# Kernel optimization log

Hardware: AMD Instinct MI355X
Metric: run time of the kernel (lower is better)

Reference implementation:

```python
import jax, jax.numpy as jnp
import numpy as np

B, L, C = 256, 256, 128
HID, H = 128, 4
D = HID // H            # 32
NUM_LAYERS = 2
NEG_SLOPE = 0.2
LN_EPS = 1e-5


def setup_inputs() -> dict:
    key = jax.random.key(0)
    ks = jax.random.split(key, 16)
    E = 4096
    x = jax.random.normal(ks[0], (B, L, C), dtype=jnp.float32)
    edge_index = jax.random.randint(ks[1], (2, E), 0, C, dtype=jnp.int64)
    s_in = 1.0 / np.sqrt(L)
    s_h = 1.0 / np.sqrt(HID)
    return {
        "x": x,
        "edge_index": edge_index,
        "emb_W": jax.random.normal(ks[2], (L, HID), jnp.float32) * s_in,
        "emb_b": jnp.zeros((HID,), jnp.float32),
        "lin_l_W": jax.random.normal(ks[3], (NUM_LAYERS, HID, HID), jnp.float32) * s_h,
        "lin_l_b": jnp.zeros((NUM_LAYERS, HID), jnp.float32),
        "lin_r_W": jax.random.normal(ks[4], (NUM_LAYERS, HID, HID), jnp.float32) * s_h,
        "lin_r_b": jnp.zeros((NUM_LAYERS, HID), jnp.float32),
        "att": jax.random.normal(ks[5], (NUM_LAYERS, H, D), jnp.float32) * (1.0 / np.sqrt(D)),
        "gat_bias": jnp.zeros((NUM_LAYERS, HID), jnp.float32),
        "ln_gamma": jnp.ones((NUM_LAYERS, HID), jnp.float32),
        "ln_beta": jnp.zeros((NUM_LAYERS, HID), jnp.float32),
        "proj_W": jax.random.normal(ks[6], (HID, L), jnp.float32) * s_h,
        "proj_b": jnp.zeros((L,), jnp.float32),
    }


def _batch_edges(edge_index):
    # replicate single-graph edges per batch sample with node offsets, then add self loops
    E = edge_index.shape[1]
    off = jnp.repeat(jnp.arange(B, dtype=edge_index.dtype) * C, E)
    src = jnp.tile(edge_index[0], B) + off
    dst = jnp.tile(edge_index[1], B) + off
    loop = jnp.arange(B * C, dtype=edge_index.dtype)
    return jnp.concatenate([src, loop]), jnp.concatenate([dst, loop])


def _layer_norm(x, g, b):
    mu = jnp.mean(x, axis=-1, keepdims=True)
    var = jnp.mean(jnp.square(x - mu), axis=-1, keepdims=True)
    return (x - mu) * jax.lax.rsqrt(var + LN_EPS) * g + b


def _gatv2(x, src, dst, Wl, bl, Wr, br, a, bias):
    N = x.shape[0]
    xl = (x @ Wl + bl).reshape(N, H, D)   # source-side transform
    xr = (x @ Wr + br).reshape(N, H, D)   # target-side transform
    e = jax.nn.leaky_relu(xl[src] + xr[dst], NEG_SLOPE)   # (E', H, D)
    logits = jnp.einsum('ehd,hd->eh', e, a)               # (E', H)
    m = jax.ops.segment_max(logits, dst, num_segments=N)
    p = jnp.exp(logits - m[dst])
    s = jax.ops.segment_sum(p, dst, num_segments=N)
    alpha = p / (s[dst] + 1e-16)
    out = jax.ops.segment_sum(xl[src] * alpha[:, :, None], dst, num_segments=N)
    return out.reshape(N, HID) + bias, alpha


def reference(x, edge_index, emb_W, emb_b, lin_l_W, lin_l_b, lin_r_W, lin_r_b,
              att, gat_bias, ln_gamma, ln_beta, proj_W, proj_b):
    src, dst = _batch_edges(edge_index)
    # (B, L, C) -> nodes are channels: (B*C, L) -> embed to HID
    h = x.transpose(0, 2, 1).reshape(B * C, L) @ emb_W + emb_b
    alpha = None
    for i in range(NUM_LAYERS):
        new_h, alpha = _gatv2(h, src, dst, lin_l_W[i], lin_l_b[i],
                              lin_r_W[i], lin_r_b[i], att[i], gat_bias[i])
        new_h = jax.nn.elu(new_h)
        h = h + new_h
        h = _layer_norm(h, ln_gamma[i], ln_beta[i])
        # dropout: eval mode, identity
    # attention map (to_dense_adj semantics: adj[b, src%C, dst%C] = mean_h(alpha), then transpose)
    b_idx = src // C
    dense = jnp.zeros((B, C, C), x.dtype).at[b_idx, src % C, dst % C].add(alpha.mean(axis=-1))
    attn_map = dense.transpose(0, 2, 1)
    out = (h @ proj_W + proj_b).reshape(B, C, L).transpose(0, 2, 1)  # (B, L, C)
    return out, attn_map
```

## Files before the change

### kernel.cpp

```cpp
#include <hip/hip_runtime.h>
#include <hip/hip_fp16.h>
#include <math.h>

#define BB 256
#define LL 256
#define CC 128
#define HIDD 128
#define HH 4
#define DD 32
#define EE 4096
#define NN (BB*CC)
#define LN_EPS 1e-5f

typedef short bf16x8 __attribute__((ext_vector_type(8)));
typedef _Float16 f16x8 __attribute__((ext_vector_type(8)));
typedef float f32x4 __attribute__((ext_vector_type(4)));

__device__ __forceinline__ float red64(float p) {
    p += __shfl_xor(p, 32);
    p += __shfl_xor(p, 16);
    p += __shfl_xor(p, 8);
    p += __shfl_xor(p, 4);
    p += __shfl_xor(p, 2);
    p += __shfl_xor(p, 1);
    return p;
}
__device__ __forceinline__ unsigned bfr(float f) {
    unsigned x = __float_as_uint(f);
    return (x + 0x7FFFu + ((x >> 16) & 1u)) >> 16;
}
__device__ __forceinline__ unsigned pack2(float a, float b) { return bfr(a) | (bfr(b) << 16); }
__device__ __forceinline__ float b2f(unsigned u) { return __uint_as_float(u << 16); }

__device__ __forceinline__ void stage_bf16_rm(ushort* lds, const ushort* src, int ldm, int t) {
    #pragma unroll
    for (int i = 0; i < 8; ++i) {
        int flat = i*256 + t;
        int r = flat >> 4, c = flat & 15;
        uint4 pk = *(const uint4*)(src + (size_t)r*ldm + c*8);
        *(uint4*)&lds[((r*16) + (c ^ (r & 7)))*8] = pk;
    }
}
__device__ __forceinline__ void mfma_tile_128(const ushort* Als, const ushort* Bls,
                                              f32x4 acc[2][8], int w, int lane) {
    int mr = lane & 15, quad = lane >> 4;
    #pragma unroll
    for (int ks = 0; ks < 4; ++ks) {
        int ca = ks*4 + quad;
        bf16x8 a[2], b[8];
        #pragma unroll
        for (int mf = 0; mf < 2; ++mf) {
            int m = w*32 + mf*16 + mr;
            a[mf] = *(const bf16x8*)&Als[((m*16) + (ca ^ (m & 7)))*8];
        }
        #pragma unroll
        for (int nf = 0; nf < 8; ++nf) {
            int n = nf*16 + mr;
            b[nf] = *(const bf16x8*)&Bls[((n*16) + (ca ^ (n & 7)))*8];
        }
        #pragma unroll
        for (int mf = 0; mf < 2; ++mf)
            #pragma unroll
            for (int nf = 0; nf < 8; ++nf)
                acc[mf][nf] = __builtin_amdgcn_mfma_f32_16x16x32_bf16(a[mf], b[nf], acc[mf][nf], 0, 0, 0);
    }
}
#define ZERO_ACC(acc) { _Pragma("unroll") for (int i_=0;i_<2;++i_) { _Pragma("unroll") for (int j_=0;j_<8;++j_) acc[i_][j_] = (f32x4){0.f,0.f,0.f,0.f}; } }

__global__ __launch_bounds__(256) void prep_weights(const float* __restrict__ emb_W,
                                                    const float* __restrict__ lWl,
                                                    const float* __restrict__ lWr,
                                                    const float* __restrict__ pW,
                                                    const int* __restrict__ edge,
                                                    ushort* __restrict__ WembT,
                                                    ushort* __restrict__ WlrT,
                                                    ushort* __restrict__ WpT,
                                                    __half* __restrict__ mult_ds) {
    __shared__ int cnt[CC*CC];
    int t = threadIdx.x;
    if (blockIdx.x == 64) {
        for (int i = t; i < CC*CC; i += 256) cnt[i] = 0;
        __syncthreads();
        for (int j = t; j < EE; j += 256) {
            int s = edge[j], d = edge[EE + j];
            atomicAdd(&cnt[s*CC + d], 1);
        }
        __syncthreads();
        for (int o = t; o < CC*CC; o += 256) {
            int dstc = o >> 7, srcc = o & 127;
            int c = cnt[srcc*CC + dstc] + ((srcc == dstc) ? 1 : 0);
            mult_ds[o] = __float2half((float)c);
        }
        return;
    }
    int gid = blockIdx.x * 256 + t;
    float v[8];
    if (gid < 4096) {
        int f = gid >> 5, ch = gid & 31;
        #pragma unroll
        for (int j = 0; j < 8; ++j) v[j] = emb_W[(size_t)(ch*8 + j)*HIDD + f];
        uint4 pk; pk.x = pack2(v[0],v[1]); pk.y = pack2(v[2],v[3]);
        pk.z = pack2(v[4],v[5]); pk.w = pack2(v[6],v[7]);
        *(uint4*)&WembT[(size_t)f*LL + ch*8] = pk;
    } else if (gid < 12288) {
        int g = gid - 4096;
        int mat = g >> 11, f = (g >> 4) & 127, ch = g & 15;
        const float* src = ((mat & 1) ? lWr : lWl) + (size_t)(mat >> 1)*HIDD*HIDD;
        #pragma unroll
        for (int j = 0; j < 8; ++j) v[j] = src[(size_t)(ch*8 + j)*HIDD + f];
        uint4 pk; pk.x = pack2(v[0],v[1]); pk.y = pack2(v[2],v[3]);
        pk.z = pack2(v[4],v[5]); pk.w = pack2(v[6],v[7]);
        *(uint4*)&WlrT[(size_t)mat*HIDD*HIDD + (size_t)f*HIDD + ch*8] = pk;
    } else {
        int g = gid - 12288;
        int l = g >> 4, ch = g & 15;
        #pragma unroll
        for (int j = 0; j < 8; ++j) v[j] = pW[(size_t)(ch*8 + j)*LL + l];
        uint4 pk; pk.x = pack2(v[0],v[1]); pk.y = pack2(v[2],v[3]);
        pk.z = pack2(v[4],v[5]); pk.w = pack2(v[6],v[7]);
        *(uint4*)&WpT[(size_t)l*HIDD + ch*8] = pk;
    }
}

__global__ __launch_bounds__(256) void embed_mfma(const float* __restrict__ x,
                                                  const ushort* __restrict__ WembT,
                                                  const float* __restrict__ bias,
                                                  ushort* __restrict__ hout) {
    __shared__ __align__(16) ushort Als[128*16*8];
    __shared__ __align__(16) ushort Bls[128*16*8];
    int b = blockIdx.x;
    int t = threadIdx.x, lane = t & 63, w = t >> 6;
    f32x4 acc[2][8];
    ZERO_ACC(acc)
    #pragma unroll
    for (int kh = 0; kh < 2; ++kh) {
        if (kh) __syncthreads();
        const float4* x4 = (const float4*)(x + (size_t)b*LL*CC + (size_t)kh*128*CC);
        int rot = (t >> 3) & 3;
        #pragma unroll
        for (int i = 0; i < 8; ++i) {
            int flat = i*256 + t;
            int lp = flat >> 5, c4 = flat & 31;
            float4 v0 = x4[(size_t)(2*lp)*32 + c4];
            float4 v1 = x4[(size_t)(2*lp + 1)*32 + c4];
            int lc = lp >> 2, lh = lp & 3;
            #pragma unroll
            for (int j0 = 0; j0 < 4; ++j0) {
                int j = (j0 + rot) & 3;
                int c = c4*4 + j;
                unsigned pk = pack2(((const float*)&v0)[j], ((const float*)&v1)[j]);
                *(unsigned*)&Als[((c*16) + (lc ^ (c & 7)))*8 + lh*2] = pk;
            }
        }
        stage_bf16_rm(Bls, WembT + kh*128, LL, t);
        __syncthreads();
        mfma_tile_128(Als, Bls, acc, w, lane);
    }
    int mr = lane & 15, quad = lane >> 4;
    #pragma unroll
    for (int nf = 0; nf < 8; ++nf) {
        int f = nf*16 + mr;
        float bv = bias[f];
        #pragma unroll
        for (int mf = 0; mf < 2; ++mf)
            #pragma unroll
            for (int r = 0; r < 4; ++r) {
                int node = w*32 + mf*16 + quad*4 + r;
                hout[((size_t)b*CC + node)*HIDD + f] = (ushort)bfr(acc[mf][nf][r] + bv);
            }
    }
}

__global__ __launch_bounds__(256) void lin_mfma(const ushort* __restrict__ hmat,
                                                const ushort* __restrict__ WlT,
                                                const ushort* __restrict__ WrT,
                                                const float* __restrict__ bl,
                                                const float* __restrict__ br,
                                                __half* __restrict__ xlT,
                                                __half* __restrict__ xrT) {
    __shared__ __align__(16) ushort Als[128*16*8];
    __shared__ __align__(16) ushort Bls[128*16*8];
    int b = blockIdx.x;
    int t = threadIdx.x, lane = t & 63, w = t >> 6;
    int mr = lane & 15, quad = lane >> 4;
    stage_bf16_rm(Als, hmat + (size_t)b*CC*HIDD, HIDD, t);
    #pragma unroll
    for (int lr = 0; lr < 2; ++lr) {
        if (lr) __syncthreads();
        stage_bf16_rm(Bls, lr ? WrT : WlT, HIDD, t);
        __syncthreads();
        f32x4 acc[2][8];
        ZERO_ACC(acc)
        mfma_tile_128(Als, Bls, acc, w, lane);
        const float* bias = lr ? br : bl;
        __half* out = lr ? xrT : xlT;
        #pragma unroll
        for (int nf = 0; nf < 8; ++nf) {
            int f = nf*16 + mr;
            float bv = bias[f];
            int h = f >> 5, d = f & 31;
            #pragma unroll
            for (int mf = 0; mf < 2; ++mf)
                #pragma unroll
                for (int r = 0; r < 4; ++r) {
                    int node = w*32 + mf*16 + quad*4 + r;
                    out[(((size_t)b*HH + h)*CC + node)*DD + d] = __float2half(acc[mf][nf][r] + bv);
                }
        }
    }
}

__global__ __launch_bounds__(256, 4) void gat_fused(const __half* __restrict__ xl_h,
                                                    const __half* __restrict__ xr_h,
                                                    const __half* __restrict__ mult_ds,
                                                    const float* __restrict__ att,
                                                    __half* __restrict__ xagg,
                                                    __half* __restrict__ Pg) {
    __shared__ __align__(16) __half xl_lds[CC*DD];
    __shared__ __align__(16) __half xlT_swz[DD*16*8];
    __shared__ float Slq[CC];
    __shared__ float rpart[4][CC];
    __shared__ float spart[4][CC];

    int bh = blockIdx.x;
    int h = bh & 3, b = bh >> 2;
    int t = threadIdx.x;
    int sg = t >> 6, dl = t & 63;
    int dstA = dl, dstB = dl + 64;

    {
        const uint4* sp = (const uint4*)(xl_h + (size_t)bh * CC * DD);
        uint4* dp = (uint4*)xl_lds;
        dp[t] = sp[t];
        dp[t + 256] = sp[t + 256];
    }
    __half2 qa2[16];
    const float* ag = att + h*DD;
    #pragma unroll
    for (int c = 0; c < 8; ++c) {
        float4 av = *(const float4*)&ag[c*4];
        qa2[2*c+0] = __floats2half2_rn(0.4f*av.x, 0.4f*av.y);
        qa2[2*c+1] = __floats2half2_rn(0.4f*av.z, 0.4f*av.w);
    }
    __half2 xrA[16], xrB[16];
    float fSA, fSB;
    {
        uint4 XA[4], XB[4];
        const uint4* pa = (const uint4*)(xr_h + ((size_t)bh*CC + dstA)*DD);
        const uint4* pb = (const uint4*)(xr_h + ((size_t)bh*CC + dstB)*DD);
        #pragma unroll
        for (int c = 0; c < 4; ++c) { XA[c] = pa[c]; XB[c] = pb[c]; }
        const __half2* va = (const __half2*)XA;
        const __half2* vb = (const __half2*)XB;
        float sA = 0.f, sB = 0.f;
        #pragma unroll
        for (int i = 0; i < 16; ++i) {
            xrA[i] = va[i]; xrB[i] = vb[i];
            __half2 p = __hmul2(qa2[i], xrA[i]);
            sA += __low2float(p) + __high2float(p);
            __half2 q = __hmul2(qa2[i], xrB[i]);
            sB += __low2float(q) + __high2float(q);
        }
        fSA = 1.5f * sA; fSB = 1.5f * sB;
    }
    __syncthreads();

    if (t < CC) {
        uint4 R[4];
        const uint4* rp = (const uint4*)&xl_lds[t*DD];
        #pragma unroll
        for (int c = 0; c < 4; ++c) R[c] = rp[c];
        const __half2* rv = (const __half2*)R;
        __half2 s = __floats2half2_rn(0.f, 0.f);
        #pragma unroll
        for (int i = 0; i < 16; ++i) s = __hfma2(qa2[i], rv[i], s);
        Slq[t] = 1.5f * (__low2float(s) + __high2float(s));
    }
    for (int i = t; i < 512; i += 256) {
        int f = i & 31, c = i >> 5;
        __align__(16) __half v[8];
        #pragma unroll
        for (int e = 0; e < 8; ++e) v[e] = xl_lds[(c*8 + e)*DD + f];
        *(uint4*)&xlT_swz[((f*16) + (c ^ (f & 7)))*8] = *(uint4*)v;
    }
    __syncthreads();

    __half2 lvA[16], lvB[16];
    float pmA0 = -3.0e38f, pmA1 = pmA0, pmB0 = pmA0, pmB1 = pmA0;
    float lbufA = 0.f, lbufB = 0.f;
    #pragma unroll
    for (int j = 0; j < 32; ++j) {
        int src = sg*32 + j;
        uint4 R[4];
        const uint4* rp = (const uint4*)&xl_lds[src*DD];
        R[0] = rp[0]; R[1] = rp[1]; R[2] = rp[2]; R[3] = rp[3];
        float sl = Slq[src];
        const __half2* xv = (const __half2*)R;
        __half2 a0 = __floats2half2_rn(0.f,0.f), a1 = a0, a2 = a0, a3 = a0;
        __half2 b0 = a0, b1 = a0, b2 = a0, b3 = a0;
        #pragma unroll
        for (int q = 0; q < 4; ++q) {
            a0 = __hfma2(qa2[4*q+0], __habs2(__hadd2(xv[4*q+0], xrA[4*q+0])), a0);
            a1 = __hfma2(qa2[4*q+1], __habs2(__hadd2(xv[4*q+1], xrA[4*q+1])), a1);
            a2 = __hfma2(qa2[4*q+2], __habs2(__hadd2(xv[4*q+2], xrA[4*q+2])), a2);
            a3 = __hfma2(qa2[4*q+3], __habs2(__hadd2(xv[4*q+3], xrA[4*q+3])), a3);
            b0 = __hfma2(qa2[4*q+0], __habs2(__hadd2(xv[4*q+0], xrB[4*q+0])), b0);
            b1 = __hfma2(qa2[4*q+1], __habs2(__hadd2(xv[4*q+1], xrB[4*q+1])), b1);
            b2 = __hfma2(qa2[4*q+2], __habs2(__hadd2(xv[4*q+2], xrB[4*q+2])), b2);
            b3 = __hfma2(qa2[4*q+3], __habs2(__hadd2(xv[4*q+3], xrB[4*q+3])), b3);
        }
        __half2 tsA = __hadd2(__hadd2(a0, a1), __hadd2(a2, a3));
        __half2 tsB = __hadd2(__hadd2(b0, b1), __hadd2(b2, b3));
        float lA = (fSA + sl) + (__low2float(tsA) + __high2float(tsA));
        float lB = (fSB + sl) + (__low2float(tsB) + __high2float(tsB));
        if (j & 1) {
            pmA1 = fmaxf(pmA1, lA); pmB1 = fmaxf(pmB1, lB);
            lvA[j >> 1] = __floats2half2_rn(lbufA, lA);
            lvB[j >> 1] = __floats2half2_rn(lbufB, lB);
        } else {
            pmA0 = fmaxf(pmA0, lA); pmB0 = fmaxf(pmB0, lB);
            lbufA = lA; lbufB = lB;
        }
    }
    rpart[sg][dstA] = fmaxf(pmA0, pmA1);
    rpart[sg][dstB] = fmaxf(pmB0, pmB1);
    __syncthreads();
    float mA = fmaxf(fmaxf(rpart[0][dstA], rpart[1][dstA]),
                     fmaxf(rpart[2][dstA], rpart[3][dstA]));
    float mB = fmaxf(fmaxf(rpart[0][dstB], rpart[1][dstB]),
                     fmaxf(rpart[2][dstB], rpart[3][dstB]));

    uint4 MAr[4], MBr[4];
    {
        const uint4* ma = (const uint4*)(mult_ds + (size_t)dstA*CC + sg*32);
        const uint4* mb = (const uint4*)(mult_ds + (size_t)dstB*CC + sg*32);
        #pragma unroll
        for (int c = 0; c < 4; ++c) { MAr[c] = ma[c]; MBr[c] = mb[c]; }
    }
    const __half* multA = (const __half*)MAr;
    const __half* multB = (const __half*)MBr;

    float sA0 = 0.f, sA1 = 0.f, sB0 = 0.f, sB1 = 0.f;
    #pragma unroll
    for (int i = 0; i < 16; ++i) {
        float eA0 = __expf(__low2float(lvA[i]) - mA) * __half2float(multA[2*i]);
        float eA1 = __expf(__high2float(lvA[i]) - mA) * __half2float(multA[2*i+1]);
        float eB0 = __expf(__low2float(lvB[i]) - mB) * __half2float(multB[2*i]);
        float eB1 = __expf(__high2float(lvB[i]) - mB) * __half2float(multB[2*i+1]);
        if (i & 1) { sA1 += eA0 + eA1; sB1 += eB0 + eB1; }
        else       { sA0 += eA0 + eA1; sB0 += eB0 + eB1; }
        lvA[i] = __floats2half2_rn(eA0, eA1);
        lvB[i] = __floats2half2_rn(eB0, eB1);
    }
    spart[sg][dstA] = sA0 + sA1;
    spart[sg][dstB] = sB0 + sB1;
    __syncthreads();
    float isA = 1.f / (((spart[0][dstA] + spart[1][dstA]) +
                        (spart[2][dstA] + spart[3][dstA])) + 1e-16f);
    float isB = 1.f / (((spart[0][dstB] + spart[1][dstB]) +
                        (spart[2][dstB] + spart[3][dstB])) + 1e-16f);

    size_t pbase = (size_t)bh * CC * CC;
    {
        int mr = dl & 15, dr0 = dl >> 4;
        __half* pA = Pg + pbase + (((size_t)(dr0*4 + sg))*64)*8;
        __half* pB = Pg + pbase + (((size_t)((dr0 + 4)*4 + sg))*64)*8;
        #pragma unroll
        for (int q = 0; q < 4; ++q) {
            int slot = mr*4 + (q ^ (mr & 3));
            __align__(16) __half ovA[8], ovB[8];
            #pragma unroll
            for (int i = 0; i < 4; ++i) {
                __half2 vA = lvA[q*4 + i], vB = lvB[q*4 + i];
                ovA[2*i+0] = __float2half(__low2float(vA) * isA);
                ovA[2*i+1] = __float2half(__high2float(vA) * isA);
                ovB[2*i+0] = __float2half(__low2float(vB) * isB);
                ovB[2*i+1] = __float2half(__high2float(vB) * isB);
            }
            *(uint4*)&pA[slot*8] = *(uint4*)ovA;
            *(uint4*)&pB[slot*8] = *(uint4*)ovB;
        }
    }
    __syncthreads();

    int quad = dl >> 4, mr = dl & 15;
    const __half* pb = Pg + pbase;
    f16x8 afr[2][4];
    #pragma unroll
    for (int mf = 0; mf < 2; ++mf) {
        int dr0 = sg*2 + mf;
        #pragma unroll
        for (int ks = 0; ks < 4; ++ks)
            afr[mf][ks] = *(const f16x8*)&pb[(((size_t)(dr0*4 + ks))*64 +
                                             mr*4 + (quad ^ (mr & 3)))*8];
    }
    f32x4 acc[2][2];
    #pragma unroll
    for (int i = 0; i < 2; ++i)
        #pragma unroll
        for (int j = 0; j < 2; ++j) acc[i][j] = (f32x4){0.f,0.f,0.f,0.f};
    #pragma unroll
    for (int ks = 0; ks < 4; ++ks) {
        int ca = ks*4 + quad;
        f16x8 bfr2[2];
        #pragma unroll
        for (int nf = 0; nf < 2; ++nf) {
            int n = nf*16 + mr;
            bfr2[nf] = *(const f16x8*)&xlT_swz[((n*16) + (ca ^ (n & 7)))*8];
        }
        #pragma unroll
        for (int mf = 0; mf < 2; ++mf)
            #pragma unroll
            for (int nf = 0; nf < 2; ++nf)
                acc[mf][nf] = __builtin_amdgcn_mfma_f32_16x16x32_f16(afr[mf][ks], bfr2[nf], acc[mf][nf], 0, 0, 0);
    }
    #pragma unroll
    for (int mf = 0; mf < 2; ++mf)
        #pragma unroll
        for (int nf = 0; nf < 2; ++nf) {
            int f = nf*16 + mr;
            #pragma unroll
            for (int r = 0; r < 4; ++r) {
                int node = sg*32 + mf*16 + quad*4 + r;
                xagg[(((size_t)b*CC + node)*HH + h)*DD + f] = __float2half(acc[mf][nf][r]);
            }
        }
}

__global__ __launch_bounds__(256) void gat_epilogue(const __half* __restrict__ xagg,
                                                    const float* __restrict__ gbias,
                                                    const float* __restrict__ ln_g,
                                                    const float* __restrict__ ln_b,
                                                    const __half* __restrict__ Pws,
                                                    ushort* __restrict__ hmat,
                                                    float* __restrict__ attn_out) {
    __shared__ float wred[4], wred2[4];
    int t = threadIdx.x;
    int nl = t >> 7, f = t & 127;
    int node = blockIdx.x*2 + nl;
    int b = node >> 7, dstc = node & 127;

    float o = __half2float(xagg[(size_t)node*HIDD + f]) + gbias[f];
    o = o > 0.f ? o : (__expf(o) - 1.f);
    float hv = b2f((unsigned)hmat[(size_t)node*HIDD + f]) + o;

    float sum = red64(hv);
    if ((t & 63) == 0) wred[t >> 6] = sum;
    __syncthreads();
    float mean = (wred[nl*2] + wred[nl*2+1]) * 0.0078125f;
    float d = hv - mean;
    float q = red64(d * d);
    if ((t & 63) == 0) wred2[t >> 6] = q;
    __syncthreads();
    float var = (wred2[nl*2] + wred2[nl*2+1]) * 0.0078125f;
    hmat[(size_t)node*HIDD + f] = (ushort)bfr(d * rsqrtf(var + LN_EPS) * ln_g[f] + ln_b[f]);

    if (attn_out) {
        int ks = f >> 5, qq = (f >> 3) & 3, e = f & 7;
        int mr = dstc & 15, dr0 = dstc >> 4;
        int slot = mr*4 + (qq ^ (mr & 3));
        size_t off = ((size_t)(dr0*4 + ks)*64 + slot)*8 + e;
        float a = 0.f;
        #pragma unroll
        for (int hh = 0; hh < HH; ++hh)
            a += __half2float(Pws[(size_t)(b*HH + hh)*CC*CC + off]);
        attn_out[(size_t)node*CC + f] = 0.25f * a;
    }
}

__global__ __launch_bounds__(256) void proj_mfma(const ushort* __restrict__ hmat,
                                                 const ushort* __restrict__ WpT,
                                                 const float* __restrict__ bias,
                                                 float* __restrict__ out) {
    __shared__ __align__(16) ushort Als[128*16*8];
    __shared__ __align__(16) ushort Bls[128*16*8];
    int l0 = blockIdx.x * 128;
    int b  = blockIdx.y;
    int t = threadIdx.x, lane = t & 63, w = t >> 6;
    f32x4 acc[2][8];
    ZERO_ACC(acc)
    stage_bf16_rm(Als, WpT + (size_t)l0*HIDD, HIDD, t);
    stage_bf16_rm(Bls, hmat + (size_t)b*CC*HIDD, HIDD, t);
    __syncthreads();
    mfma_tile_128(Als, Bls, acc, w, lane);
    int mr = lane & 15, quad = lane >> 4;
    #pragma unroll
    for (int nf = 0; nf < 8; ++nf) {
        int c = nf*16 + mr;
        #pragma unroll
        for (int mf = 0; mf < 2; ++mf)
            #pragma unroll
            for (int r = 0; r < 4; ++r) {
                int l = l0 + w*32 + mf*16 + quad*4 + r;
                out[((size_t)b*LL + l)*CC + c] = acc[mf][nf][r] + bias[l];
            }
    }
}

extern "C" void kernel_launch(void* const* d_in, const int* in_sizes, int n_in,
                              void* d_out, int out_size, void* d_ws, size_t ws_size,
                              hipStream_t stream) {
    const float* x        = (const float*)d_in[0];
    const int*   edge     = (const int*)d_in[1];
    const float* emb_W    = (const float*)d_in[2];
    const float* emb_b    = (const float*)d_in[3];
    const float* lin_l_W  = (const float*)d_in[4];
    const float* lin_l_b  = (const float*)d_in[5];
    const float* lin_r_W  = (const float*)d_in[6];
    const float* lin_r_b  = (const float*)d_in[7];
    const float* att      = (const float*)d_in[8];
    const float* gat_bias = (const float*)d_in[9];
    const float* ln_g     = (const float*)d_in[10];
    const float* ln_b     = (const float*)d_in[11];
    const float* proj_W   = (const float*)d_in[12];
    const float* proj_b   = (const float*)d_in[13];

    ushort* h     = (ushort*)d_ws;
    __half* xl_h  = (__half*)(h + (size_t)NN * HIDD);
    __half* xr_h  = xl_h + (size_t)NN * HIDD;
    __half* xagg  = xr_h + (size_t)NN * HIDD;
    __half* Pg    = xagg + (size_t)NN * HIDD;
    __half* mult_ds = Pg + (size_t)BB * HH * CC * CC;
    ushort* WembT = (ushort*)(mult_ds + (size_t)CC * CC);
    ushort* WlrT  = WembT + (size_t)CC*LL;
    ushort* WpT   = WlrT + (size_t)4*HIDD*HIDD;

    float* out0 = (float*)d_out;
    float* attn = out0 + (size_t)BB * LL * CC;

    prep_weights<<<65, 256, 0, stream>>>(emb_W, lin_l_W, lin_r_W, proj_W, edge,
                                         WembT, WlrT, WpT, mult_ds);
    embed_mfma<<<BB, 256, 0, stream>>>(x, WembT, emb_b, h);
    for (int layer = 0; layer < 2; ++layer) {
        lin_mfma<<<BB, 256, 0, stream>>>(h,
            WlrT + (size_t)(layer*2 + 0)*HIDD*HIDD,
            WlrT + (size_t)(layer*2 + 1)*HIDD*HIDD,
            lin_l_b + layer*HIDD, lin_r_b + layer*HIDD,
            xl_h, xr_h);
        gat_fused<<<BB*HH, 256, 0, stream>>>(xl_h, xr_h, mult_ds,
            att + layer*HIDD, xagg, Pg);
        gat_epilogue<<<NN/2, 256, 0, stream>>>(xagg,
            gat_bias + layer*HIDD, ln_g + layer*HIDD, ln_b + layer*HIDD,
            (layer == 1) ? Pg : nullptr, h, (layer == 1) ? attn : nullptr);
    }
    proj_mfma<<<dim3(2, BB), 256, 0, stream>>>(h, WpT, proj_b, out0);
}
```

Baseline: 307.1 us.

## Keep attention matrix in LDS, write P to global only on last layer

```diff
diff --git a/kernel.cpp b/kernel.cpp
--- a/kernel.cpp
+++ b/kernel.cpp
@@ -210,17 +210,22 @@
     }
 }
 
-__global__ __launch_bounds__(256, 4) void gat_fused(const __half* __restrict__ xl_h,
-                                                    const __half* __restrict__ xr_h,
-                                                    const __half* __restrict__ mult_ds,
-                                                    const float* __restrict__ att,
-                                                    __half* __restrict__ xagg,
-                                                    __half* __restrict__ Pg) {
-    __shared__ __align__(16) __half xl_lds[CC*DD];
+#define SLOT(q, mr) ((mr)*4 + (((q) ^ (mr) ^ ((mr) >> 2)) & 3))
+
+__global__ __launch_bounds__(256) __attribute__((amdgpu_waves_per_eu(4, 4)))
+void gat_fused(const __half* __restrict__ xl_h,
+               const __half* __restrict__ xr_h,
+               const __half* __restrict__ mult_ds,
+               const float* __restrict__ att,
+               __half* __restrict__ xagg,
+               __half* __restrict__ Pg) {
+    __shared__ __align__(16) __half smemA[CC*CC];
     __shared__ __align__(16) __half xlT_swz[DD*16*8];
-    __shared__ float Slq[CC];
-    __shared__ float rpart[4][CC];
-    __shared__ float spart[4][CC];
+    __half* xl_lds = smemA;
+    float*  Slq    = (float*)(smemA + CC*DD);
+    float*  rp     = Slq + CC;
+    float*  sp     = rp + 4*CC;
+    __half* Pfrag  = smemA;
 
     int bh = blockIdx.x;
     int h = bh & 3, b = bh >> 2;
@@ -229,10 +234,10 @@
     int dstA = dl, dstB = dl + 64;
 
     {
-        const uint4* sp = (const uint4*)(xl_h + (size_t)bh * CC * DD);
+        const uint4* spg = (const uint4*)(xl_h + (size_t)bh * CC * DD);
         uint4* dp = (uint4*)xl_lds;
-        dp[t] = sp[t];
-        dp[t + 256] = sp[t + 256];
+        dp[t] = spg[t];
+        dp[t + 256] = spg[t + 256];
     }
     __half2 qa2[16];
     const float* ag = att + h*DD;
@@ -267,9 +272,9 @@
 
     if (t < CC) {
         uint4 R[4];
-        const uint4* rp = (const uint4*)&xl_lds[t*DD];
-        #pragma unroll
-        for (int c = 0; c < 4; ++c) R[c] = rp[c];
+        const uint4* rpt = (const uint4*)&xl_lds[t*DD];
+        #pragma unroll
+        for (int c = 0; c < 4; ++c) R[c] = rpt[c];
         const __half2* rv = (const __half2*)R;
         __half2 s = __floats2half2_rn(0.f, 0.f);
         #pragma unroll
@@ -292,8 +297,8 @@
     for (int j = 0; j < 32; ++j) {
         int src = sg*32 + j;
         uint4 R[4];
-        const uint4* rp = (const uint4*)&xl_lds[src*DD];
-        R[0] = rp[0]; R[1] = rp[1]; R[2] = rp[2]; R[3] = rp[3];
+        const uint4* rpt = (const uint4*)&xl_lds[src*DD];
+        R[0] = rpt[0]; R[1] = rpt[1]; R[2] = rpt[2]; R[3] = rpt[3];
         float sl = Slq[src];
         const __half2* xv = (const __half2*)R;
         __half2 a0 = __floats2half2_rn(0.f,0.f), a1 = a0, a2 = a0, a3 = a0;
@@ -322,13 +327,13 @@
             lbufA = lA; lbufB = lB;
         }
     }
-    rpart[sg][dstA] = fmaxf(pmA0, pmA1);
-    rpart[sg][dstB] = fmaxf(pmB0, pmB1);
-    __syncthreads();
-    float mA = fmaxf(fmaxf(rpart[0][dstA], rpart[1][dstA]),
-                     fmaxf(rpart[2][dstA], rpart[3][dstA]));
-    float mB = fmaxf(fmaxf(rpart[0][dstB], rpart[1][dstB]),
-                     fmaxf(rpart[2][dstB], rpart[3][dstB]));
+    rp[sg*CC + dstA] = fmaxf(pmA0, pmA1);
+    rp[sg*CC + dstB] = fmaxf(pmB0, pmB1);
+    __syncthreads();
+    float mA = fmaxf(fmaxf(rp[0*CC + dstA], rp[1*CC + dstA]),
+                     fmaxf(rp[2*CC + dstA], rp[3*CC + dstA]));
+    float mB = fmaxf(fmaxf(rp[0*CC + dstB], rp[1*CC + dstB]),
+                     fmaxf(rp[2*CC + dstB], rp[3*CC + dstB]));
 
     uint4 MAr[4], MBr[4];
     {
@@ -352,22 +357,23 @@
         lvA[i] = __floats2half2_rn(eA0, eA1);
         lvB[i] = __floats2half2_rn(eB0, eB1);
     }
-    spart[sg][dstA] = sA0 + sA1;
-    spart[sg][dstB] = sB0 + sB1;
-    __syncthreads();
-    float isA = 1.f / (((spart[0][dstA] + spart[1][dstA]) +
-                        (spart[2][dstA] + spart[3][dstA])) + 1e-16f);
-    float isB = 1.f / (((spart[0][dstB] + spart[1][dstB]) +
-                        (spart[2][dstB] + spart[3][dstB])) + 1e-16f);
-
-    size_t pbase = (size_t)bh * CC * CC;
+    sp[sg*CC + dstA] = sA0 + sA1;
+    sp[sg*CC + dstB] = sB0 + sB1;
+    __syncthreads();
+    float isA = 1.f / (((sp[0*CC + dstA] + sp[1*CC + dstA]) +
+                        (sp[2*CC + dstA] + sp[3*CC + dstA])) + 1e-16f);
+    float isB = 1.f / (((sp[0*CC + dstB] + sp[1*CC + dstB]) +
+                        (sp[2*CC + dstB] + sp[3*CC + dstB])) + 1e-16f);
+    __syncthreads();
+
     {
         int mr = dl & 15, dr0 = dl >> 4;
-        __half* pA = Pg + pbase + (((size_t)(dr0*4 + sg))*64)*8;
-        __half* pB = Pg + pbase + (((size_t)((dr0 + 4)*4 + sg))*64)*8;
+        __half* pfA = &Pfrag[(((dr0    )*4 + sg)*64)*8];
+        __half* pfB = &Pfrag[(((dr0 + 4)*4 + sg)*64)*8];
+        __half* pgA = Pg ? Pg + (size_t)bh*CC*CC + (size_t)dstA*CC + sg*32 : nullptr;
+        __half* pgB = Pg ? Pg + (size_t)bh*CC*CC + (size_t)dstB*CC + sg*32 : nullptr;
         #pragma unroll
         for (int q = 0; q < 4; ++q) {
-            int slot = mr*4 + (q ^ (mr & 3));
             __align__(16) __half ovA[8], ovB[8];
             #pragma unroll
             for (int i = 0; i < 4; ++i) {
@@ -377,22 +383,24 @@
                 ovB[2*i+0] = __float2half(__low2float(vB) * isB);
                 ovB[2*i+1] = __float2half(__high2float(vB) * isB);
             }
-            *(uint4*)&pA[slot*8] = *(uint4*)ovA;
-            *(uint4*)&pB[slot*8] = *(uint4*)ovB;
+            *(uint4*)&pfA[SLOT(q, mr)*8] = *(uint4*)ovA;
+            *(uint4*)&pfB[SLOT(q, mr)*8] = *(uint4*)ovB;
+            if (pgA) {
+                *(uint4*)&pgA[q*8] = *(uint4*)ovA;
+                *(uint4*)&pgB[q*8] = *(uint4*)ovB;
+            }
         }
     }
     __syncthreads();
 
     int quad = dl >> 4, mr = dl & 15;
-    const __half* pb = Pg + pbase;
     f16x8 afr[2][4];
     #pragma unroll
     for (int mf = 0; mf < 2; ++mf) {
         int dr0 = sg*2 + mf;
         #pragma unroll
         for (int ks = 0; ks < 4; ++ks)
-            afr[mf][ks] = *(const f16x8*)&pb[(((size_t)(dr0*4 + ks))*64 +
-                                             mr*4 + (quad ^ (mr & 3)))*8];
+            afr[mf][ks] = *(const f16x8*)&Pfrag[((dr0*4 + ks)*64 + SLOT(quad, mr))*8];
     }
     f32x4 acc[2][2];
     #pragma unroll
@@ -434,37 +442,41 @@
                                                     const __half* __restrict__ Pws,
                                                     ushort* __restrict__ hmat,
                                                     float* __restrict__ attn_out) {
-    __shared__ float wred[4], wred2[4];
     int t = threadIdx.x;
-    int nl = t >> 7, f = t & 127;
-    int node = blockIdx.x*2 + nl;
+    int w = t >> 6, lane = t & 63;
+    int node = blockIdx.x*4 + w;
     int b = node >> 7, dstc = node & 127;
-
-    float o = __half2float(xagg[(size_t)node*HIDD + f]) + gbias[f];
-    o = o > 0.f ? o : (__expf(o) - 1.f);
-    float hv = b2f((unsigned)hmat[(size_t)node*HIDD + f]) + o;
-
-    float sum = red64(hv);
-    if ((t & 63) == 0) wred[t >> 6] = sum;
-    __syncthreads();
-    float mean = (wred[nl*2] + wred[nl*2+1]) * 0.0078125f;
-    float d = hv - mean;
-    float q = red64(d * d);
-    if ((t & 63) == 0) wred2[t >> 6] = q;
-    __syncthreads();
-    float var = (wred2[nl*2] + wred2[nl*2+1]) * 0.0078125f;
-    hmat[(size_t)node*HIDD + f] = (ushort)bfr(d * rsqrtf(var + LN_EPS) * ln_g[f] + ln_b[f]);
+    int f0 = lane*2;
+
+    __half2 xa = *(const __half2*)&xagg[(size_t)node*HIDD + f0];
+    unsigned hp = *(const unsigned*)&hmat[(size_t)node*HIDD + f0];
+    float2 gb = *(const float2*)&gbias[f0];
+    float o0 = __low2float(xa) + gb.x;
+    float o1 = __high2float(xa) + gb.y;
+    o0 = o0 > 0.f ? o0 : (__expf(o0) - 1.f);
+    o1 = o1 > 0.f ? o1 : (__expf(o1) - 1.f);
+    float hv0 = b2f(hp & 0xFFFFu) + o0;
+    float hv1 = b2f(hp >> 16) + o1;
+
+    float mean = red64(hv0 + hv1) * 0.0078125f;
+    float d0 = hv0 - mean, d1 = hv1 - mean;
+    float var = red64(d0*d0 + d1*d1) * 0.0078125f;
+    float rs = rsqrtf(var + LN_EPS);
+    float2 g2 = *(const float2*)&ln_g[f0];
+    float2 be = *(const float2*)&ln_b[f0];
+    *(unsigned*)&hmat[(size_t)node*HIDD + f0] =
+        pack2(d0*rs*g2.x + be.x, d1*rs*g2.y + be.y);
 
     if (attn_out) {
-        int ks = f >> 5, qq = (f >> 3) & 3, e = f & 7;
-        int mr = dstc & 15, dr0 = dstc >> 4;
-        int slot = mr*4 + (qq ^ (mr & 3));
-        size_t off = ((size_t)(dr0*4 + ks)*64 + slot)*8 + e;
-        float a = 0.f;
-        #pragma unroll
-        for (int hh = 0; hh < HH; ++hh)
-            a += __half2float(Pws[(size_t)(b*HH + hh)*CC*CC + off]);
-        attn_out[(size_t)node*CC + f] = 0.25f * a;
+        float a0 = 0.f, a1 = 0.f;
+        #pragma unroll
+        for (int hh = 0; hh < HH; ++hh) {
+            __half2 v = *(const __half2*)&Pws[((size_t)(b*HH + hh)*CC + dstc)*CC + f0];
+            a0 += __low2float(v);
+            a1 += __high2float(v);
+        }
+        float2 o; o.x = 0.25f*a0; o.y = 0.25f*a1;
+        *(float2*)&attn_out[(size_t)node*CC + f0] = o;
     }
 }
 
@@ -538,8 +550,8 @@
             lin_l_b + layer*HIDD, lin_r_b + layer*HIDD,
             xl_h, xr_h);
         gat_fused<<<BB*HH, 256, 0, stream>>>(xl_h, xr_h, mult_ds,
-            att + layer*HIDD, xagg, Pg);
-        gat_epilogue<<<NN/2, 256, 0, stream>>>(xagg,
+            att + layer*HIDD, xagg, (layer == 1) ? Pg : nullptr);
+        gat_epilogue<<<NN/4, 256, 0, stream>>>(xagg,
             gat_bias + layer*HIDD, ln_g + layer*HIDD, ln_b + layer*HIDD,
             (layer == 1) ? Pg : nullptr, h, (layer == 1) ? attn : nullptr);
     }
```

Measured after the change: 288.3 us. 1.07x faster.
